# Kernel tuning notes

Measured on AMD Instinct MI355X. Metric: run time of the kernel, lower is better.

The kernel has to match this reference:

```python
import jax, jax.numpy as jnp
import numpy as np

B, N, T = 64, 1024, 512  # batch, node_num (= input_dim = hidden_dim), seq_len


def setup_inputs() -> dict:
    key = jax.random.key(0)
    k0, k1, k2, k3, k4 = jax.random.split(key, 5)
    flow_x = jax.random.normal(k0, (B, N, T, 1), dtype=jnp.float32)
    s = 1.0 / np.sqrt(N)  # torch nn.Linear default init bound
    W1 = jax.random.uniform(k1, (N, 2 * N), jnp.float32, -s, s)
    b1 = jax.random.uniform(k2, (2 * N,), jnp.float32, -s, s)
    W2 = jax.random.uniform(k3, (N, N), jnp.float32, -s, s)
    b2 = jax.random.uniform(k4, (N,), jnp.float32, -s, s)
    return {"flow_x": flow_x, "W1": W1, "b1": b1, "W2": W2, "b2": b2}


def reference(flow_x, W1, b1, W2, b2):
    Bs, Nn, Ts, _ = flow_x.shape
    # [B, N, T, 1] -> [B, T, N]
    x = jnp.transpose(flow_x, (0, 2, 1, 3)).reshape(Bs, Ts, Nn)
    # Precompute input projections for all timesteps (batched GEMM)
    xp = x @ W1 + b1                      # [B, T, 2N]
    xh = x @ W2 + b2                      # [B, T, N]
    x1, x2 = jnp.split(xp, 2, axis=-1)    # each [B, T, N]

    def step(h, inp):
        x1t, x2t, xht = inp               # each [B, N]
        hp = h @ W1 + b1                  # [B, 2N]
        h1, h2 = jnp.split(hp, 2, axis=-1)
        z = jax.nn.sigmoid(x1t + h1)
        r = jax.nn.sigmoid(x2t + h2)
        h_hat = jnp.tanh(xht + r * (h @ W2 + b2))
        h_new = z * h + (1.0 - z) * h_hat
        return h_new, None

    h0 = jnp.zeros((Bs, Nn), dtype=x.dtype)
    xs = (jnp.swapaxes(x1, 0, 1), jnp.swapaxes(x2, 0, 1), jnp.swapaxes(xh, 0, 1))
    hT, _ = jax.lax.scan(step, h0, xs)
    # original returns last output reshaped to [B, N, 1, 1]
    return hT.reshape(Bs, Nn, 1, 1)
```

## Files before the change

kernel.cpp:

```cpp
#include <hip/hip_runtime.h>


#define BATCH 64
#define NN 1024
#define TSTEPS 512
#define HB_ELEMS ((size_t)BATCH * NN)

typedef __attribute__((ext_vector_type(8))) short short8;
typedef __attribute__((ext_vector_type(8))) unsigned short u16x8;
typedef __attribute__((ext_vector_type(4))) unsigned short u16x4;
typedef __attribute__((ext_vector_type(4))) float f32x4;

#define MFMA16(a, b, c) __builtin_amdgcn_mfma_f32_16x16x32_bf16((a), (b), (c), 0, 0, 0)

__device__ __forceinline__ unsigned short f2bf(float x) {
  union { float f; unsigned u; } v; v.f = x;
  unsigned u = v.u + 0x7FFFu + ((v.u >> 16) & 1u);
  return (unsigned short)(u >> 16);
}
__device__ __forceinline__ float bf2f(unsigned short h) {
  union { unsigned u; float f; } v; v.u = ((unsigned)h) << 16; return v.f;
}

__global__ void trans_x(const float* __restrict__ fx, unsigned short* __restrict__ xT) {
  int bid = blockIdx.x;
  int b   = bid >> 7;
  int rem = bid & 127;
  int kt  = rem >> 3;
  int tt  = rem & 7;
  __shared__ float tl[64][65];
  int tx = threadIdx.x & 63;
  int ty = threadIdx.x >> 6;
  const float* src = fx + ((size_t)(b * NN + kt * 64)) * TSTEPS + tt * 64;
#pragma unroll
  for (int i = 0; i < 16; i++) {
    int kr = i * 4 + ty;
    tl[kr][tx] = src[(size_t)kr * TSTEPS + tx];
  }
  __syncthreads();
#pragma unroll
  for (int i = 0; i < 16; i++) {
    int tr = i * 4 + ty;
    xT[((size_t)((tt * 64 + tr) * 64 + b)) * NN + kt * 64 + tx] = f2bf(tl[tx][tr]);
  }
}

__global__ void prep_w(const float* __restrict__ W1, const float* __restrict__ W2,
                       unsigned short* __restrict__ wt) {
  int bid = blockIdx.x;
  int s    = bid >> 8;
  int tile = bid & 255;
  int kt = tile >> 4, jt = tile & 15;
  const float* src = (s < 2) ? W1 : W2;
  int ld = (s < 2) ? 2048 : 1024;
  int co = (s == 1) ? 1024 : 0;
  __shared__ float tl[64][65];
  int tx = threadIdx.x & 63, ty = threadIdx.x >> 6;
#pragma unroll
  for (int i = 0; i < 16; i++) {
    int kr = i * 4 + ty;
    tl[kr][tx] = src[(size_t)(kt * 64 + kr) * ld + co + jt * 64 + tx];
  }
  __syncthreads();
#pragma unroll
  for (int i = 0; i < 16; i++) {
    int jr = i * 4 + ty;
    wt[((size_t)(s * NN + jt * 64 + jr)) * NN + kt * 64 + tx] = f2bf(tl[tx][jr]);
  }
}

__global__ __launch_bounds__(256) void precompute(
    const unsigned short* __restrict__ xT, const unsigned short* __restrict__ wt,
    const float* __restrict__ b1, const float* __restrict__ b2,
    unsigned short* __restrict__ P2) {
  int m0 = (blockIdx.x / 24) * 128;
  int n0 = (blockIdx.x % 24) * 128;
  __shared__ unsigned short As[128 * 40];
  __shared__ unsigned short Bs[128 * 40];
  int tid = threadIdx.x;
  int wave = tid >> 6, lane = tid & 63, q = lane >> 4, li = lane & 15;
  int wm = wave >> 1, wn = wave & 1;
  f32x4 acc[4][4];
#pragma unroll
  for (int a = 0; a < 4; a++)
#pragma unroll
    for (int b = 0; b < 4; b++) acc[a][b] = (f32x4)(0.f);

  for (int kk = 0; kk < 32; ++kk) {
    int K0 = kk * 32;
#pragma unroll
    for (int e = 0; e < 2; e++) {
      int c = tid * 2 + e;
      int row = c >> 2, part = c & 3;
      *(u16x8*)&As[row * 40 + part * 8] =
          *(const u16x8*)&xT[(size_t)(m0 + row) * NN + K0 + part * 8];
      *(u16x8*)&Bs[row * 40 + part * 8] =
          *(const u16x8*)&wt[(size_t)(n0 + row) * NN + K0 + part * 8];
    }
    __syncthreads();
    short8 af[4], bfr[4];
#pragma unroll
    for (int mt = 0; mt < 4; mt++)
      af[mt] = *(const short8*)&As[(wm * 64 + mt * 16 + li) * 40 + q * 8];
#pragma unroll
    for (int nt = 0; nt < 4; nt++)
      bfr[nt] = *(const short8*)&Bs[(wn * 64 + nt * 16 + li) * 40 + q * 8];
#pragma unroll
    for (int mt = 0; mt < 4; mt++)
#pragma unroll
      for (int nt = 0; nt < 4; nt++)
        acc[mt][nt] = MFMA16(af[mt], bfr[nt], acc[mt][nt]);
    __syncthreads();
  }
#pragma unroll
  for (int mt = 0; mt < 4; mt++) {
    int m = m0 + wm * 64 + mt * 16 + q * 4;
    int t = m >> 6, b = m & 63;
#pragma unroll
    for (int nt = 0; nt < 4; nt++) {
      int n = n0 + wn * 64 + nt * 16 + li;
      float bias = (n < 2048) ? b1[n] : b2[n - 2048];
      int s = n >> 10, j = n & 1023;
      f32x4 a = acc[mt][nt];
      u16x4 pk;
      pk.x = f2bf(a.x + bias); pk.y = f2bf(a.y + bias);
      pk.z = f2bf(a.z + bias); pk.w = f2bf(a.w + bias);
      *(u16x4*)&P2[(((size_t)t * 3 + s) * NN + j) * 64 + b] = pk;
    }
  }
}

#define AL(p)    __hip_atomic_load((p),  __ATOMIC_RELAXED, __HIP_MEMORY_SCOPE_AGENT)
#define AS(p, v) __hip_atomic_store((p), (v), __ATOMIC_RELAXED, __HIP_MEMORY_SCOPE_AGENT)

__global__ __launch_bounds__(256, 1) void gru_scan(
    unsigned short* __restrict__ hb, const unsigned short* __restrict__ wt,
    const unsigned short* __restrict__ P2,
    const float* __restrict__ b1, const float* __restrict__ b2,
    float* __restrict__ out, unsigned* __restrict__ cnt) {
  int bid = blockIdx.x;
  int jt = bid & 63, mq = bid >> 6;
  int j0 = jt * 16, m0 = mq * 16;
  int tid = threadIdx.x, wave = tid >> 6, lane = tid & 63, q = lane >> 4, li = lane & 15;
  int kb = wave * 256;

  const short8* Bz = (const short8*)&wt[((size_t)(0 * NN + j0 + li)) * NN + kb + q * 8];
  const short8* Br = (const short8*)&wt[((size_t)(1 * NN + j0 + li)) * NN + kb + q * 8];
  const short8* Bv = (const short8*)&wt[((size_t)(2 * NN + j0 + li)) * NN + kb + q * 8];
  short8 wz[8], wr[8], wv[8];
#pragma unroll
  for (int r = 0; r < 8; r++) {
    wz[r] = Bz[r * 4];
    wr[r] = Br[r * 4];
    wv[r] = Bv[r * 4];
  }

  int j = j0 + li;
  int bbase = m0 + q * 4;
  float b1z = b1[j], b1r = b1[NN + j], b2v = b2[j];
  const unsigned short* pz = &P2[((size_t)0 * NN + j) * 64 + bbase];
  const unsigned short* pr = &P2[((size_t)1 * NN + j) * 64 + bbase];
  const unsigned short* pv = &P2[((size_t)2 * NN + j) * 64 + bbase];
  const size_t pstride = (size_t)3 * NN * 64;

  unsigned* poll_w = &cnt[(mq * 4 + wave) * 64];
  unsigned* arr_w  = &cnt[(mq * 4 + (jt >> 4)) * 64];

  const size_t aoff = (size_t)(m0 + li) * 256 + wave * 64 + q * 2;

  f32x4 hc = (f32x4)(0.f);
  __shared__ f32x4 red[9][64];

  for (int t = 0; t < TSTEPS; t++) {
    u16x4 pz4, pr4, pv4;
    if (wave == 0) {
      pz4 = *(const u16x4*)pz;
      pr4 = *(const u16x4*)pr;
      pv4 = *(const u16x4*)pv;
    }
    if (t > 0) {
      unsigned target = 16u * (unsigned)t;
      while (AL(poll_w) < target) __builtin_amdgcn_s_sleep(1);
    }
    const unsigned long long* hin =
        (const unsigned long long*)(hb + ((size_t)(t & 3)) * HB_ELEMS);
    union { unsigned long long u[2]; short8 s; } fa[8];
#pragma unroll
    for (int r = 0; r < 8; r++) {
      fa[r].u[0] = AL(hin + aoff + r * 8);
      fa[r].u[1] = AL(hin + aoff + r * 8 + 1);
    }
    f32x4 az = (f32x4)(0.f), ar = (f32x4)(0.f), av = (f32x4)(0.f);
#pragma unroll
    for (int r = 0; r < 8; r++) {
      az = MFMA16(fa[r].s, wz[r], az);
      ar = MFMA16(fa[r].s, wr[r], ar);
      av = MFMA16(fa[r].s, wv[r], av);
    }
    if (wave > 0) {
      red[(wave - 1) * 3 + 0][lane] = az;
      red[(wave - 1) * 3 + 1][lane] = ar;
      red[(wave - 1) * 3 + 2][lane] = av;
    }
    __syncthreads();
    if (wave == 0) {
#pragma unroll
      for (int w = 0; w < 3; w++) {
        az += red[w * 3 + 0][lane];
        ar += red[w * 3 + 1][lane];
        av += red[w * 3 + 2][lane];
      }
#pragma unroll
      for (int reg = 0; reg < 4; reg++) {
        float z = 1.f / (1.f + __expf(-(az[reg] + bf2f(pz4[reg]) + b1z)));
        float r = 1.f / (1.f + __expf(-(ar[reg] + bf2f(pr4[reg]) + b1r)));
        float x = bf2f(pv4[reg]) + r * (av[reg] + b2v);
        float e = __expf(-2.f * fabsf(x));
        float th = (1.f - e) / (1.f + e);
        float hh = (x >= 0.f) ? th : -th;
        hc[reg] = z * hc[reg] + (1.f - z) * hh;
      }
      if (t < TSTEPS - 1) {
        unsigned* hout = (unsigned*)(hb + ((size_t)((t + 1) & 3)) * HB_ELEMS);
#pragma unroll
        for (int reg = 0; reg < 4; reg++) {
          unsigned mine = f2bf(hc[reg]);
          unsigned other = (unsigned)__shfl_xor((int)mine, 1, 64);
          if ((lane & 1) == 0) {
            unsigned packed = mine | (other << 16);
            AS(&hout[(size_t)(bbase + reg) * (NN / 2) + (j >> 1)], packed);
          }
        }
        asm volatile("s_waitcnt vmcnt(0)" ::: "memory");
        if (lane == 0)
          __hip_atomic_fetch_add(arr_w, 1u, __ATOMIC_RELAXED,
                                 __HIP_MEMORY_SCOPE_AGENT);
      }
    }
    pz += pstride; pr += pstride; pv += pstride;
  }

  if (wave == 0) {
#pragma unroll
    for (int reg = 0; reg < 4; reg++)
      out[(size_t)(bbase + reg) * NN + j] = hc[reg];
  }
}

extern "C" void kernel_launch(void* const* d_in, const int* in_sizes, int n_in,
                              void* d_out, int out_size, void* d_ws, size_t ws_size,
                              hipStream_t stream) {
  const float* flow_x = (const float*)d_in[0];
  const float* W1 = (const float*)d_in[1];
  const float* b1 = (const float*)d_in[2];
  const float* W2 = (const float*)d_in[3];
  const float* b2 = (const float*)d_in[4];
  float* out = (float*)d_out;
  char* ws = (char*)d_ws;
  size_t off = 0;
  auto take = [&](size_t bytes) -> char* {
    char* p = ws + off;
    off += (bytes + 255) & ~(size_t)255;
    return p;
  };
  unsigned short* wt  = (unsigned short*)take((size_t)3 * 1024 * 1024 * 2);
  unsigned short* xT  = (unsigned short*)take((size_t)32768 * 1024 * 2);
  unsigned short* P2  = (unsigned short*)take((size_t)512 * 3 * 1024 * 64 * 2);
  unsigned short* hb  = (unsigned short*)take((size_t)4 * HB_ELEMS * 2);
  unsigned*       cnt = (unsigned*)take((size_t)16 * 64 * 4);

  if (off > ws_size) {
    hipMemsetAsync(d_out, 0, (size_t)out_size * 4, stream);
    return;
  }

  hipMemsetAsync(hb, 0, HB_ELEMS * 2, stream);
  hipMemsetAsync(cnt, 0, (size_t)16 * 64 * 4, stream);

  prep_w<<<768, 256, 0, stream>>>(W1, W2, wt);
  trans_x<<<8192, 256, 0, stream>>>(flow_x, xT);
  precompute<<<6144, 256, 0, stream>>>(xT, wt, b1, b2, P2);

  void* args[] = {&hb, &wt, &P2, &b1, &b2, &out, &cnt};
  hipLaunchCooperativeKernel((const void*)gru_scan, dim3(256), dim3(256),
                             args, 0, stream);
}
```

Baseline: 3.567 ms.

## Replace atomic counter barrier with per-block step flags and move weights to LDS

Each block's step barrier switches from spinning on one shared atomic counter incremented by 16 producers to polling 16 per-producer flags, one lane each, set by exchange to the step number. This targets contention and serialization on the counter atomics. Recurrent weights move from registers into LDS, which frees VGPRs but adds LDS reads every step. Hidden-state stores become 64-bit exchanges, halving the number of store instructions.

```diff
diff --git a/kernel.cpp b/kernel.cpp
--- a/kernel.cpp
+++ b/kernel.cpp
@@ -130,30 +130,30 @@
   }
 }
 
-#define AL(p)    __hip_atomic_load((p),  __ATOMIC_RELAXED, __HIP_MEMORY_SCOPE_AGENT)
-#define AS(p, v) __hip_atomic_store((p), (v), __ATOMIC_RELAXED, __HIP_MEMORY_SCOPE_AGENT)
+#define AL(p)      __hip_atomic_load((p),  __ATOMIC_RELAXED, __HIP_MEMORY_SCOPE_AGENT)
+#define AXCHG(p,v) __hip_atomic_exchange((p), (v), __ATOMIC_RELAXED, __HIP_MEMORY_SCOPE_AGENT)
 
 __global__ __launch_bounds__(256, 1) void gru_scan(
     unsigned short* __restrict__ hb, const unsigned short* __restrict__ wt,
     const unsigned short* __restrict__ P2,
     const float* __restrict__ b1, const float* __restrict__ b2,
-    float* __restrict__ out, unsigned* __restrict__ cnt) {
+    float* __restrict__ out, unsigned* __restrict__ flags) {
   int bid = blockIdx.x;
   int jt = bid & 63, mq = bid >> 6;
   int j0 = jt * 16, m0 = mq * 16;
   int tid = threadIdx.x, wave = tid >> 6, lane = tid & 63, q = lane >> 4, li = lane & 15;
   int kb = wave * 256;
 
-  const short8* Bz = (const short8*)&wt[((size_t)(0 * NN + j0 + li)) * NN + kb + q * 8];
-  const short8* Br = (const short8*)&wt[((size_t)(1 * NN + j0 + li)) * NN + kb + q * 8];
-  const short8* Bv = (const short8*)&wt[((size_t)(2 * NN + j0 + li)) * NN + kb + q * 8];
-  short8 wz[8], wr[8], wv[8];
-#pragma unroll
-  for (int r = 0; r < 8; r++) {
-    wz[r] = Bz[r * 4];
-    wr[r] = Br[r * 4];
-    wv[r] = Bv[r * 4];
-  }
+  __shared__ unsigned short wlds[49152];
+  __shared__ f32x4 red[9][64];
+  int wq = (li * 4 + q) * 8;
+#pragma unroll
+  for (int g = 0; g < 3; g++)
+#pragma unroll
+    for (int r = 0; r < 8; r++)
+      *(u16x8*)&wlds[((wave * 3 + g) * 8 + r) * 512 + wq] =
+          *(const u16x8*)&wt[((size_t)(g * NN + j0 + li)) * NN + kb + r * 32 + q * 8];
+  __syncthreads();
 
   int j = j0 + li;
   int bbase = m0 + q * 4;
@@ -163,13 +163,12 @@
   const unsigned short* pv = &P2[((size_t)2 * NN + j) * 64 + bbase];
   const size_t pstride = (size_t)3 * NN * 64;
 
-  unsigned* poll_w = &cnt[(mq * 4 + wave) * 64];
-  unsigned* arr_w  = &cnt[(mq * 4 + (jt >> 4)) * 64];
+  unsigned* poll_w = &flags[(mq * 4 + wave) * 16 + (lane & 15)];
+  unsigned* flag_w = &flags[(mq * 4 + (jt >> 4)) * 16 + (jt & 15)];
 
   const size_t aoff = (size_t)(m0 + li) * 256 + wave * 64 + q * 2;
 
   f32x4 hc = (f32x4)(0.f);
-  __shared__ f32x4 red[9][64];
 
   for (int t = 0; t < TSTEPS; t++) {
     u16x4 pz4, pr4, pv4;
@@ -179,8 +178,11 @@
       pv4 = *(const u16x4*)pv;
     }
     if (t > 0) {
-      unsigned target = 16u * (unsigned)t;
-      while (AL(poll_w) < target) __builtin_amdgcn_s_sleep(1);
+      for (;;) {
+        unsigned v = AL(poll_w);
+        if (!__any((int)v < t)) break;
+        __builtin_amdgcn_s_sleep(1);
+      }
     }
     const unsigned long long* hin =
         (const unsigned long long*)(hb + ((size_t)(t & 3)) * HB_ELEMS);
@@ -193,9 +195,10 @@
     f32x4 az = (f32x4)(0.f), ar = (f32x4)(0.f), av = (f32x4)(0.f);
 #pragma unroll
     for (int r = 0; r < 8; r++) {
-      az = MFMA16(fa[r].s, wz[r], az);
-      ar = MFMA16(fa[r].s, wr[r], ar);
-      av = MFMA16(fa[r].s, wv[r], av);
+      short8 a = fa[r].s;
+      az = MFMA16(a, *(const short8*)&wlds[((wave * 3 + 0) * 8 + r) * 512 + wq], az);
+      ar = MFMA16(a, *(const short8*)&wlds[((wave * 3 + 1) * 8 + r) * 512 + wq], ar);
+      av = MFMA16(a, *(const short8*)&wlds[((wave * 3 + 2) * 8 + r) * 512 + wq], av);
     }
     if (wave > 0) {
       red[(wave - 1) * 3 + 0][lane] = az;
@@ -221,20 +224,22 @@
         hc[reg] = z * hc[reg] + (1.f - z) * hh;
       }
       if (t < TSTEPS - 1) {
-        unsigned* hout = (unsigned*)(hb + ((size_t)((t + 1) & 3)) * HB_ELEMS);
+        unsigned long long* hout =
+            (unsigned long long*)(hb + ((size_t)((t + 1) & 3)) * HB_ELEMS);
 #pragma unroll
         for (int reg = 0; reg < 4; reg++) {
           unsigned mine = f2bf(hc[reg]);
           unsigned other = (unsigned)__shfl_xor((int)mine, 1, 64);
-          if ((lane & 1) == 0) {
-            unsigned packed = mine | (other << 16);
-            AS(&hout[(size_t)(bbase + reg) * (NN / 2) + (j >> 1)], packed);
+          unsigned pair = mine | (other << 16);
+          unsigned pair2 = (unsigned)__shfl_xor((int)pair, 2, 64);
+          if ((li & 3) == 0) {
+            unsigned long long w64 =
+                (unsigned long long)pair | ((unsigned long long)pair2 << 32);
+            AXCHG(&hout[(size_t)(bbase + reg) * 256 + (j >> 2)], w64);
           }
         }
         asm volatile("s_waitcnt vmcnt(0)" ::: "memory");
-        if (lane == 0)
-          __hip_atomic_fetch_add(arr_w, 1u, __ATOMIC_RELAXED,
-                                 __HIP_MEMORY_SCOPE_AGENT);
+        if (lane == 0) AXCHG(flag_w, (unsigned)(t + 1));
       }
     }
     pz += pstride; pr += pstride; pv += pstride;
@@ -263,11 +268,11 @@
     off += (bytes + 255) & ~(size_t)255;
     return p;
   };
-  unsigned short* wt  = (unsigned short*)take((size_t)3 * 1024 * 1024 * 2);
-  unsigned short* xT  = (unsigned short*)take((size_t)32768 * 1024 * 2);
-  unsigned short* P2  = (unsigned short*)take((size_t)512 * 3 * 1024 * 64 * 2);
-  unsigned short* hb  = (unsigned short*)take((size_t)4 * HB_ELEMS * 2);
-  unsigned*       cnt = (unsigned*)take((size_t)16 * 64 * 4);
+  unsigned short* wt   = (unsigned short*)take((size_t)3 * 1024 * 1024 * 2);
+  unsigned short* xT   = (unsigned short*)take((size_t)32768 * 1024 * 2);
+  unsigned short* P2   = (unsigned short*)take((size_t)512 * 3 * 1024 * 64 * 2);
+  unsigned short* hb   = (unsigned short*)take((size_t)4 * HB_ELEMS * 2);
+  unsigned*       flags= (unsigned*)take((size_t)16 * 16 * 4);
 
   if (off > ws_size) {
     hipMemsetAsync(d_out, 0, (size_t)out_size * 4, stream);
@@ -275,13 +280,13 @@
   }
 
   hipMemsetAsync(hb, 0, HB_ELEMS * 2, stream);
-  hipMemsetAsync(cnt, 0, (size_t)16 * 64 * 4, stream);
+  hipMemsetAsync(flags, 0, (size_t)16 * 16 * 4, stream);
 
   prep_w<<<768, 256, 0, stream>>>(W1, W2, wt);
   trans_x<<<8192, 256, 0, stream>>>(flow_x, xT);
   precompute<<<6144, 256, 0, stream>>>(xT, wt, b1, b2, P2);
 
-  void* args[] = {&hb, &wt, &P2, &b1, &b2, &out, &cnt};
+  void* args[] = {&hb, &wt, &P2, &b1, &b2, &out, &flags};
   hipLaunchCooperativeKernel((const void*)gru_scan, dim3(256), dim3(256),
                              args, 0, stream);
 }
```

Measured after the change: 3.842 ms. +7.7%, slower.
